# Kernel tuning notes

Measured on AMD Instinct MI355X. Metric: run time of the kernel, lower is better.

## Reference

```python
import jax, jax.numpy as jnp
import numpy as np
from jax import lax

B = 32768
L = 200          # window_size
K = 5            # conv kernel
CIN = 6
FLAT = L - K + 1  # 196, conv1d valid output length (out channels = 1)


def setup_inputs() -> dict:
    key = jax.random.key(0)
    ks = jax.random.split(key, 9)
    s = lambda *sh: 1.0 / np.sqrt(sh[-1])
    x = jax.random.normal(ks[0], (B, CIN, L), dtype=jnp.float32)
    conv_w = jax.random.normal(ks[1], (1, CIN, K), dtype=jnp.float32) * (1.0 / np.sqrt(CIN * K))
    conv_b = jax.random.normal(ks[2], (1,), dtype=jnp.float32) * 0.1
    w1 = jax.random.normal(ks[3], (FLAT, 50), dtype=jnp.float32) * (1.0 / np.sqrt(FLAT))
    b1 = jax.random.normal(ks[4], (50,), dtype=jnp.float32) * 0.1
    w2 = jax.random.normal(ks[5], (50, 30), dtype=jnp.float32) * (1.0 / np.sqrt(50))
    b2 = jax.random.normal(ks[6], (30,), dtype=jnp.float32) * 0.1
    w3 = jax.random.normal(ks[7], (30, 15), dtype=jnp.float32) * (1.0 / np.sqrt(30))
    b3 = jax.random.normal(ks[8], (15,), dtype=jnp.float32) * 0.1
    return {"x": x, "conv_w": conv_w, "conv_b": conv_b, "w1": w1, "b1": b1,
            "w2": w2, "b2": b2, "w3": w3, "b3": b3}


def reference(x, conv_w, conv_b, w1, b1, w2, b2, w3, b3):
    # conv1d (valid): [B,6,200] -> [B,1,196]
    y = lax.conv_general_dilated(x, conv_w, window_strides=(1,), padding='VALID',
                                 dimension_numbers=('NCH', 'OIH', 'NCH'))
    y = y + conv_b[None, :, None]
    h = y.reshape(x.shape[0], -1)                       # [B,196]
    h = jax.nn.relu(h @ w1 + b1)                        # [B,50]
    h = jax.nn.relu(h @ w2 + b2)                        # [B,30]
    out = h @ w3 + b3                                   # [B,15]
    # Procrustes orthogonalization of the 3x3 block
    R = out[:, :9].reshape(-1, 3, 3)
    U, _, VT = jnp.linalg.svd(R)                        # batched 3x3 SVD
    det = jnp.linalg.det(jnp.matmul(U, VT))             # [B]
    scale = jnp.stack([jnp.ones_like(det), jnp.ones_like(det), det], axis=1)  # diag(1,1,det)
    R_norm = jnp.matmul(U, VT * scale[:, :, None])      # U @ S @ VT
    return jnp.concatenate([R_norm.reshape(-1, 9), out[:, 9:]], axis=1)
```

## Files before the change

### kernel.cpp

```cpp
#include <hip/hip_runtime.h>
#include <math.h>

#define BATCH 32768
#define LW    200
#define CIN   6
#define KSZ   5
#define FLAT  196
#define NH1   50
#define NH2   30
#define NOUT  15

#define NS    28
#define NLD   8
#define TW    33

__global__ __launch_bounds__(448) void fused_kernel(
    const float* __restrict__ x,
    const float* __restrict__ cw, const float* __restrict__ cb,
    const float* __restrict__ w1, const float* __restrict__ b1,
    const float* __restrict__ w2, const float* __restrict__ b2,
    const float* __restrict__ w3, const float* __restrict__ b3,
    float* __restrict__ out)
{
    __shared__ float xs[7 * 64 * TW];

    const int tid  = threadIdx.x;
    const int wv   = __builtin_amdgcn_readfirstlane(tid >> 6);
    const int lane = tid & 63;
    const int b    = blockIdx.x * 64 + lane;
    const int kstart = NS * wv;

    float* tile = xs + wv * (64 * TW);

    float w[CIN][KSZ];
#pragma unroll
    for (int c = 0; c < CIN; ++c)
#pragma unroll
        for (int k = 0; k < KSZ; ++k) w[c][k] = cw[c * KSZ + k];
    const float bias = cb[0];

    int goff[NLD];
    int loff[NLD];
#pragma unroll
    for (int u = 0; u < NLD; ++u) {
        int g   = lane + 64 * u;
        int row = g >> 3;
        int c4  = g & 7;
        goff[u] = row * (CIN * LW) + 4 * c4;
        loff[u] = row * TW + 4 * c4;
    }
    const float* xw = x + (size_t)blockIdx.x * 64 * (CIN * LW) + kstart;

    float acc[NS];
#pragma unroll
    for (int i = 0; i < NS; ++i) acc[i] = bias;

    float4 buf[NLD];
#pragma unroll
    for (int u = 0; u < NLD; ++u)
        buf[u] = *(const float4*)(xw + goff[u]);

#pragma unroll
    for (int ch = 0; ch < CIN; ++ch) {
#pragma unroll
        for (int u = 0; u < NLD; ++u) {
            float* dst = tile + loff[u];
            dst[0] = buf[u].x; dst[1] = buf[u].y; dst[2] = buf[u].z; dst[3] = buf[u].w;
        }
        if (ch + 1 < CIN) {
#pragma unroll
            for (int u = 0; u < NLD; ++u)
                buf[u] = *(const float4*)(xw + (ch + 1) * LW + goff[u]);
        }
        const float* row = tile + lane * TW;
        float x0 = row[0], x1 = row[1], x2 = row[2], x3 = row[3];
#pragma unroll
        for (int i = 0; i < NS; ++i) {
            float x4v = row[i + 4];
            float a = acc[i];
            a = fmaf(x0, w[ch][0], a);
            a = fmaf(x1, w[ch][1], a);
            a = fmaf(x2, w[ch][2], a);
            a = fmaf(x3, w[ch][3], a);
            a = fmaf(x4v, w[ch][4], a);
            acc[i] = a;
            x0 = x1; x1 = x2; x2 = x3; x3 = x4v;
        }
    }

    float h1p[NH1];
#pragma unroll
    for (int j = 0; j < NH1; ++j) h1p[j] = 0.f;
#pragma unroll
    for (int ii = 0; ii < NS; ++ii) {
        const float* wrow = w1 + (size_t)(kstart + ii) * NH1;
        float c = acc[ii];
#pragma unroll
        for (int j = 0; j < NH1; ++j) h1p[j] = fmaf(c, wrow[j], h1p[j]);
    }

    __syncthreads();
    float* part = xs;
    if (wv >= 4) {
#pragma unroll
        for (int j = 0; j < NH1; ++j)
            part[(wv - 4) * (64 * 53) + lane * 53 + j] = h1p[j];
    }
    __syncthreads();
    if (wv < 3) {
#pragma unroll
        for (int j = 0; j < NH1; ++j)
            h1p[j] += part[wv * (64 * 53) + lane * 53 + j];
    }
    __syncthreads();
    if (wv >= 1 && wv < 4) {
#pragma unroll
        for (int j = 0; j < NH1; ++j)
            part[(wv - 1) * (64 * 53) + lane * 53 + j] = h1p[j];
    }
    __syncthreads();
    if (wv != 0) return;

    float h1[NH1];
#pragma unroll
    for (int j = 0; j < NH1; ++j) {
        float s = h1p[j]
                + part[lane * 53 + j]
                + part[64 * 53 + lane * 53 + j]
                + part[2 * 64 * 53 + lane * 53 + j]
                + b1[j];
        h1[j] = fmaxf(s, 0.f);
    }

    float h2[NH2];
#pragma unroll
    for (int j = 0; j < NH2; ++j) h2[j] = b2[j];
#pragma unroll
    for (int k = 0; k < NH1; ++k) {
        float hk = h1[k];
        const float* row = w2 + k * NH2;
#pragma unroll
        for (int j = 0; j < NH2; ++j) h2[j] = fmaf(hk, row[j], h2[j]);
    }
#pragma unroll
    for (int j = 0; j < NH2; ++j) h2[j] = fmaxf(h2[j], 0.f);

    float o[NOUT];
#pragma unroll
    for (int j = 0; j < NOUT; ++j) o[j] = b3[j];
#pragma unroll
    for (int k = 0; k < NH2; ++k) {
        float hk = h2[k];
        const float* row = w3 + k * NOUT;
#pragma unroll
        for (int j = 0; j < NOUT; ++j) o[j] = fmaf(hk, row[j], o[j]);
    }

    {
        float r00 = o[0], r01 = o[1], r02 = o[2];
        float r10 = o[3], r11 = o[4], r12 = o[5];
        float r20 = o[6], r21 = o[7], r22 = o[8];

        float A[4][4], V[4][4];
        A[0][0] = r00 + r11 + r22;
        A[1][1] = r00 - r11 - r22;
        A[2][2] = r11 - r00 - r22;
        A[3][3] = r22 - r00 - r11;
        A[0][1] = A[1][0] = r21 - r12;
        A[0][2] = A[2][0] = r02 - r20;
        A[0][3] = A[3][0] = r10 - r01;
        A[1][2] = A[2][1] = r01 + r10;
        A[1][3] = A[3][1] = r02 + r20;
        A[2][3] = A[3][2] = r12 + r21;
#pragma unroll
        for (int i = 0; i < 4; ++i)
#pragma unroll
            for (int j = 0; j < 4; ++j) V[i][j] = (i == j) ? 1.f : 0.f;

        const int pr[6][2] = {{0,1},{0,2},{0,3},{1,2},{1,3},{2,3}};
        for (int sweep = 0; sweep < 7; ++sweep) {
#pragma unroll
            for (int pi = 0; pi < 6; ++pi) {
                const int p = pr[pi][0], q = pr[pi][1];
                float apq = A[p][q];
                if (fabsf(apq) > 1e-20f) {
                    float theta = (A[q][q] - A[p][p]) / (2.f * apq);
                    float t = copysignf(1.f, theta) / (fabsf(theta) + sqrtf(1.f + theta * theta));
                    float c = rsqrtf(1.f + t * t);
                    float s = t * c;
#pragma unroll
                    for (int k = 0; k < 4; ++k) {
                        float akp = A[k][p], akq = A[k][q];
                        A[k][p] = c * akp - s * akq;
                        A[k][q] = s * akp + c * akq;
                    }
#pragma unroll
                    for (int k = 0; k < 4; ++k) {
                        float apk = A[p][k], aqk = A[q][k];
                        A[p][k] = c * apk - s * aqk;
                        A[q][k] = s * apk + c * aqk;
                    }
#pragma unroll
                    for (int k = 0; k < 4; ++k) {
                        float vkp = V[k][p], vkq = V[k][q];
                        V[k][p] = c * vkp - s * vkq;
                        V[k][q] = s * vkp + c * vkq;
                    }
                }
            }
        }

        int best = 0;
        float bl = A[0][0];
#pragma unroll
        for (int i = 1; i < 4; ++i)
            if (A[i][i] > bl) { bl = A[i][i]; best = i; }

        float vw = V[0][best], vx = V[1][best], vy = V[2][best], vz = V[3][best];
        float inv = rsqrtf(vw * vw + vx * vx + vy * vy + vz * vz);
        vw *= inv; vx *= inv; vy *= inv; vz *= inv;

        float xx = vx * vx, yy = vy * vy, zz = vz * vz;
        float xy = vx * vy, xz = vx * vz, yz = vy * vz;
        float wx = vw * vx, wy = vw * vy, wz = vw * vz;

        float* ob = out + (long)b * NOUT;
        ob[0]  = 1.f - 2.f * (yy + zz);
        ob[1]  = 2.f * (xy - wz);
        ob[2]  = 2.f * (xz + wy);
        ob[3]  = 2.f * (xy + wz);
        ob[4]  = 1.f - 2.f * (xx + zz);
        ob[5]  = 2.f * (yz - wx);
        ob[6]  = 2.f * (xz - wy);
        ob[7]  = 2.f * (yz + wx);
        ob[8]  = 1.f - 2.f * (xx + yy);
        ob[9]  = o[9];
        ob[10] = o[10];
        ob[11] = o[11];
        ob[12] = o[12];
        ob[13] = o[13];
        ob[14] = o[14];
    }
}

extern "C" void kernel_launch(void* const* d_in, const int* in_sizes, int n_in,
                              void* d_out, int out_size, void* d_ws, size_t ws_size,
                              hipStream_t stream) {
    const float* x  = (const float*)d_in[0];
    const float* cw = (const float*)d_in[1];
    const float* cb = (const float*)d_in[2];
    const float* w1 = (const float*)d_in[3];
    const float* b1 = (const float*)d_in[4];
    const float* w2 = (const float*)d_in[5];
    const float* b2 = (const float*)d_in[6];
    const float* w3 = (const float*)d_in[7];
    const float* b3 = (const float*)d_in[8];
    float* outp = (float*)d_out;

    fused_kernel<<<BATCH / 64, 448, 0, stream>>>(x, cw, cb, w1, b1, w2, b2, w3, b3, outp);
}
```

Baseline: 319.8 us.

## Split fused kernel into single-wave conv/fc1 blocks plus separate tail kernel

Replaces the 448-thread fused block, where six of seven waves idled during the MLP and SVD tail, with two kernels. A 64-thread conv+fc1 kernel computes partial hidden sums per slice and writes them to workspace, and a separate tail kernel reduces the partials and runs fc2/fc3 and the quaternion Procrustes step. Block indices are swizzled across 8 groups. The aim is to remove the intra-block LDS reduction and the barriers, and to let the serial tail run at higher occupancy. The cost is a global round trip for the partial sums (up to 7x50xB floats) and an extra kernel launch.

New measurement: 334.7 us. +4.7%, slower.

```diff
diff --git a/kernel.cpp b/kernel.cpp
--- a/kernel.cpp
+++ b/kernel.cpp
@@ -10,27 +10,26 @@
 #define NH2   30
 #define NOUT  15
 
-#define NS    28
-#define NLD   8
-#define TW    33
-
-__global__ __launch_bounds__(448) void fused_kernel(
+
+template<int NS, int TB, int COLS, int NLD, int TW, int NSPLIT, int MINW>
+__global__ __launch_bounds__(64, MINW) void conv_fc1_kernel(
     const float* __restrict__ x,
     const float* __restrict__ cw, const float* __restrict__ cb,
-    const float* __restrict__ w1, const float* __restrict__ b1,
-    const float* __restrict__ w2, const float* __restrict__ b2,
-    const float* __restrict__ w3, const float* __restrict__ b3,
-    float* __restrict__ out)
+    const float* __restrict__ w1,
+    float* __restrict__ part)
 {
-    __shared__ float xs[7 * 64 * TW];
-
-    const int tid  = threadIdx.x;
-    const int wv   = __builtin_amdgcn_readfirstlane(tid >> 6);
-    const int lane = tid & 63;
-    const int b    = blockIdx.x * 64 + lane;
-    const int kstart = NS * wv;
-
-    float* tile = xs + wv * (64 * TW);
+    __shared__ float tile[64 * TW];
+
+    const int lane = threadIdx.x;
+    const int bid  = blockIdx.x;
+    const int r = bid & 7;
+    const int q = bid >> 3;
+    const int g = r * 64 + q / NSPLIT;
+    const int s = q - (q / NSPLIT) * NSPLIT;
+
+    const int kstart = NS * s;
+    const int tbase  = TB * s;
+    const int off    = kstart - tbase;
 
     float w[CIN][KSZ];
 #pragma unroll
@@ -43,13 +42,13 @@
     int loff[NLD];
 #pragma unroll
     for (int u = 0; u < NLD; ++u) {
-        int g   = lane + 64 * u;
-        int row = g >> 3;
-        int c4  = g & 7;
+        int g4  = lane + 64 * u;
+        int row = g4 / NLD;
+        int c4  = g4 - row * NLD;
         goff[u] = row * (CIN * LW) + 4 * c4;
         loff[u] = row * TW + 4 * c4;
     }
-    const float* xw = x + (size_t)blockIdx.x * 64 * (CIN * LW) + kstart;
+    const float* xw = x + (size_t)g * 64 * (CIN * LW) + tbase;
 
     float acc[NS];
 #pragma unroll
@@ -72,7 +71,7 @@
             for (int u = 0; u < NLD; ++u)
                 buf[u] = *(const float4*)(xw + (ch + 1) * LW + goff[u]);
         }
-        const float* row = tile + lane * TW;
+        const float* row = tile + lane * TW + off;
         float x0 = row[0], x1 = row[1], x2 = row[2], x3 = row[3];
 #pragma unroll
         for (int i = 0; i < NS; ++i) {
@@ -99,37 +98,32 @@
         for (int j = 0; j < NH1; ++j) h1p[j] = fmaf(c, wrow[j], h1p[j]);
     }
 
-    __syncthreads();
-    float* part = xs;
-    if (wv >= 4) {
-#pragma unroll
-        for (int j = 0; j < NH1; ++j)
-            part[(wv - 4) * (64 * 53) + lane * 53 + j] = h1p[j];
-    }
-    __syncthreads();
-    if (wv < 3) {
-#pragma unroll
-        for (int j = 0; j < NH1; ++j)
-            h1p[j] += part[wv * (64 * 53) + lane * 53 + j];
-    }
-    __syncthreads();
-    if (wv >= 1 && wv < 4) {
-#pragma unroll
-        for (int j = 0; j < NH1; ++j)
-            part[(wv - 1) * (64 * 53) + lane * 53 + j] = h1p[j];
-    }
-    __syncthreads();
-    if (wv != 0) return;
+    float* pb = part + (size_t)(s * NH1) * BATCH + (size_t)g * 64 + lane;
+#pragma unroll
+    for (int j = 0; j < NH1; ++j)
+        pb[(size_t)j * BATCH] = h1p[j];
+}
+
+template<int NSPLIT>
+__global__ __launch_bounds__(64, 2) void tail_kernel(
+    const float* __restrict__ part,
+    const float* __restrict__ b1,
+    const float* __restrict__ w2, const float* __restrict__ b2,
+    const float* __restrict__ w3, const float* __restrict__ b3,
+    float* __restrict__ out)
+{
+    const int bid = blockIdx.x;
+    const int g   = (bid & 7) * 64 + (bid >> 3);
+    const int b   = g * 64 + threadIdx.x;
 
     float h1[NH1];
 #pragma unroll
     for (int j = 0; j < NH1; ++j) {
-        float s = h1p[j]
-                + part[lane * 53 + j]
-                + part[64 * 53 + lane * 53 + j]
-                + part[2 * 64 * 53 + lane * 53 + j]
-                + b1[j];
-        h1[j] = fmaxf(s, 0.f);
+        float a = b1[j];
+#pragma unroll
+        for (int s = 0; s < NSPLIT; ++s)
+            a += part[(size_t)(s * NH1 + j) * BATCH + b];
+        h1[j] = fmaxf(a, 0.f);
     }
 
     float h2[NH2];
@@ -156,91 +150,89 @@
         for (int j = 0; j < NOUT; ++j) o[j] = fmaf(hk, row[j], o[j]);
     }
 
-    {
-        float r00 = o[0], r01 = o[1], r02 = o[2];
-        float r10 = o[3], r11 = o[4], r12 = o[5];
-        float r20 = o[6], r21 = o[7], r22 = o[8];
-
-        float A[4][4], V[4][4];
-        A[0][0] = r00 + r11 + r22;
-        A[1][1] = r00 - r11 - r22;
-        A[2][2] = r11 - r00 - r22;
-        A[3][3] = r22 - r00 - r11;
-        A[0][1] = A[1][0] = r21 - r12;
-        A[0][2] = A[2][0] = r02 - r20;
-        A[0][3] = A[3][0] = r10 - r01;
-        A[1][2] = A[2][1] = r01 + r10;
-        A[1][3] = A[3][1] = r02 + r20;
-        A[2][3] = A[3][2] = r12 + r21;
-#pragma unroll
-        for (int i = 0; i < 4; ++i)
-#pragma unroll
-            for (int j = 0; j < 4; ++j) V[i][j] = (i == j) ? 1.f : 0.f;
-
-        const int pr[6][2] = {{0,1},{0,2},{0,3},{1,2},{1,3},{2,3}};
-        for (int sweep = 0; sweep < 7; ++sweep) {
-#pragma unroll
-            for (int pi = 0; pi < 6; ++pi) {
-                const int p = pr[pi][0], q = pr[pi][1];
-                float apq = A[p][q];
-                if (fabsf(apq) > 1e-20f) {
-                    float theta = (A[q][q] - A[p][p]) / (2.f * apq);
-                    float t = copysignf(1.f, theta) / (fabsf(theta) + sqrtf(1.f + theta * theta));
-                    float c = rsqrtf(1.f + t * t);
-                    float s = t * c;
-#pragma unroll
-                    for (int k = 0; k < 4; ++k) {
-                        float akp = A[k][p], akq = A[k][q];
-                        A[k][p] = c * akp - s * akq;
-                        A[k][q] = s * akp + c * akq;
-                    }
-#pragma unroll
-                    for (int k = 0; k < 4; ++k) {
-                        float apk = A[p][k], aqk = A[q][k];
-                        A[p][k] = c * apk - s * aqk;
-                        A[q][k] = s * apk + c * aqk;
-                    }
-#pragma unroll
-                    for (int k = 0; k < 4; ++k) {
-                        float vkp = V[k][p], vkq = V[k][q];
-                        V[k][p] = c * vkp - s * vkq;
-                        V[k][q] = s * vkp + c * vkq;
-                    }
+    float r00 = o[0], r01 = o[1], r02 = o[2];
+    float r10 = o[3], r11 = o[4], r12 = o[5];
+    float r20 = o[6], r21 = o[7], r22 = o[8];
+
+    float A[4][4], V[4][4];
+    A[0][0] = r00 + r11 + r22;
+    A[1][1] = r00 - r11 - r22;
+    A[2][2] = r11 - r00 - r22;
+    A[3][3] = r22 - r00 - r11;
+    A[0][1] = A[1][0] = r21 - r12;
+    A[0][2] = A[2][0] = r02 - r20;
+    A[0][3] = A[3][0] = r10 - r01;
+    A[1][2] = A[2][1] = r01 + r10;
+    A[1][3] = A[3][1] = r02 + r20;
+    A[2][3] = A[3][2] = r12 + r21;
+#pragma unroll
+    for (int i = 0; i < 4; ++i)
+#pragma unroll
+        for (int j = 0; j < 4; ++j) V[i][j] = (i == j) ? 1.f : 0.f;
+
+    const int pr[6][2] = {{0,1},{0,2},{0,3},{1,2},{1,3},{2,3}};
+    for (int sweep = 0; sweep < 7; ++sweep) {
+#pragma unroll
+        for (int pi = 0; pi < 6; ++pi) {
+            const int p = pr[pi][0], qq = pr[pi][1];
+            float apq = A[p][qq];
+            if (fabsf(apq) > 1e-20f) {
+                float theta = (A[qq][qq] - A[p][p]) / (2.f * apq);
+                float t = copysignf(1.f, theta) / (fabsf(theta) + sqrtf(1.f + theta * theta));
+                float c = rsqrtf(1.f + t * t);
+                float sn = t * c;
+#pragma unroll
+                for (int k = 0; k < 4; ++k) {
+                    float akp = A[k][p], akq = A[k][qq];
+                    A[k][p] = c * akp - sn * akq;
+                    A[k][qq] = sn * akp + c * akq;
+                }
+#pragma unroll
+                for (int k = 0; k < 4; ++k) {
+                    float apk = A[p][k], aqk = A[qq][k];
+                    A[p][k] = c * apk - sn * aqk;
+                    A[qq][k] = sn * apk + c * aqk;
+                }
+#pragma unroll
+                for (int k = 0; k < 4; ++k) {
+                    float vkp = V[k][p], vkq = V[k][qq];
+                    V[k][p] = c * vkp - sn * vkq;
+                    V[k][qq] = sn * vkp + c * vkq;
                 }
             }
         }
-
-        int best = 0;
-        float bl = A[0][0];
-#pragma unroll
-        for (int i = 1; i < 4; ++i)
-            if (A[i][i] > bl) { bl = A[i][i]; best = i; }
-
-        float vw = V[0][best], vx = V[1][best], vy = V[2][best], vz = V[3][best];
-        float inv = rsqrtf(vw * vw + vx * vx + vy * vy + vz * vz);
-        vw *= inv; vx *= inv; vy *= inv; vz *= inv;
-
-        float xx = vx * vx, yy = vy * vy, zz = vz * vz;
-        float xy = vx * vy, xz = vx * vz, yz = vy * vz;
-        float wx = vw * vx, wy = vw * vy, wz = vw * vz;
-
-        float* ob = out + (long)b * NOUT;
-        ob[0]  = 1.f - 2.f * (yy + zz);
-        ob[1]  = 2.f * (xy - wz);
-        ob[2]  = 2.f * (xz + wy);
-        ob[3]  = 2.f * (xy + wz);
-        ob[4]  = 1.f - 2.f * (xx + zz);
-        ob[5]  = 2.f * (yz - wx);
-        ob[6]  = 2.f * (xz - wy);
-        ob[7]  = 2.f * (yz + wx);
-        ob[8]  = 1.f - 2.f * (xx + yy);
-        ob[9]  = o[9];
-        ob[10] = o[10];
-        ob[11] = o[11];
-        ob[12] = o[12];
-        ob[13] = o[13];
-        ob[14] = o[14];
-    }
+    }
+
+    int best = 0;
+    float bl = A[0][0];
+#pragma unroll
+    for (int i = 1; i < 4; ++i)
+        if (A[i][i] > bl) { bl = A[i][i]; best = i; }
+
+    float vw = V[0][best], vx = V[1][best], vy = V[2][best], vz = V[3][best];
+    float inv = rsqrtf(vw * vw + vx * vx + vy * vy + vz * vz);
+    vw *= inv; vx *= inv; vy *= inv; vz *= inv;
+
+    float xx = vx * vx, yy = vy * vy, zz = vz * vz;
+    float xy = vx * vy, xz = vx * vz, yz = vy * vz;
+    float wx = vw * vx, wy = vw * vy, wz = vw * vz;
+
+    float* ob = out + (long)b * NOUT;
+    ob[0]  = 1.f - 2.f * (yy + zz);
+    ob[1]  = 2.f * (xy - wz);
+    ob[2]  = 2.f * (xz + wy);
+    ob[3]  = 2.f * (xy + wz);
+    ob[4]  = 1.f - 2.f * (xx + zz);
+    ob[5]  = 2.f * (yz - wx);
+    ob[6]  = 2.f * (xz - wy);
+    ob[7]  = 2.f * (yz + wx);
+    ob[8]  = 1.f - 2.f * (xx + yy);
+    ob[9]  = o[9];
+    ob[10] = o[10];
+    ob[11] = o[11];
+    ob[12] = o[12];
+    ob[13] = o[13];
+    ob[14] = o[14];
 }
 
 extern "C" void kernel_launch(void* const* d_in, const int* in_sizes, int n_in,
@@ -256,6 +248,22 @@
     const float* w3 = (const float*)d_in[7];
     const float* b3 = (const float*)d_in[8];
     float* outp = (float*)d_out;
-
-    fused_kernel<<<BATCH / 64, 448, 0, stream>>>(x, cw, cb, w1, b1, w2, b2, w3, b3, outp);
+    float* part = (float*)d_ws;
+
+    const size_t need7 = (size_t)7 * NH1 * BATCH * sizeof(float);
+    const size_t need4 = (size_t)4 * NH1 * BATCH * sizeof(float);
+
+    if (ws_size >= need7) {
+        conv_fc1_kernel<28, 28, 32, 8, 33, 7, 4>
+            <<<7 * (BATCH / 64), 64, 0, stream>>>(x, cw, cb, w1, part);
+        tail_kernel<7><<<BATCH / 64, 64, 0, stream>>>(part, b1, w2, b2, w3, b3, outp);
+    } else if (ws_size >= need4) {
+        conv_fc1_kernel<49, 48, 56, 14, 57, 4, 3>
+            <<<4 * (BATCH / 64), 64, 0, stream>>>(x, cw, cb, w1, part);
+        tail_kernel<4><<<BATCH / 64, 64, 0, stream>>>(part, b1, w2, b2, w3, b3, outp);
+    } else {
+        conv_fc1_kernel<98, 96, 104, 26, 105, 2, 1>
+            <<<2 * (BATCH / 64), 64, 0, stream>>>(x, cw, cb, w1, part);
+        tail_kernel<2><<<BATCH / 64, 64, 0, stream>>>(part, b1, w2, b2, w3, b3, outp);
+    }
 }
```
